# Kernel tuning notes

Measured on AMD Instinct MI355X. Metric: run time of the kernel, lower is better.

## Reference

```python
import jax, jax.numpy as jnp
import numpy as np
from jax import lax

NUM_WORDS, WORD_DIM = 50000, 300
NUM_CHARS, CHAR_DIM = 100, 100
NUM_POS, POS_DIM = 50, 100
NUM_FILTERS, KERNEL = 100, 3
PRIVACY_TERMS = (3, 7, 11)


def setup_inputs() -> dict:
    key = jax.random.key(0)
    ks = jax.random.split(key, 8)
    bs, ls, cl = 64, 512, 32
    return {
        "input_word": jax.random.randint(ks[0], (bs, ls), 0, NUM_WORDS, dtype=jnp.int64 if jax.config.jax_enable_x64 else jnp.int32),
        "input_char": jax.random.randint(ks[1], (bs, ls, cl), 0, NUM_CHARS),
        "input_pos": jax.random.randint(ks[2], (bs, ls), 0, NUM_POS),
        "word_table": jax.random.normal(ks[3], (NUM_WORDS, WORD_DIM), jnp.float32) * 0.1,
        "char_table": jax.random.normal(ks[4], (NUM_CHARS, CHAR_DIM), jnp.float32) * 0.1,
        "pos_table": jax.random.normal(ks[5], (NUM_POS, POS_DIM), jnp.float32) * 0.1,
        "conv_w": jax.random.normal(ks[6], (NUM_FILTERS, CHAR_DIM, KERNEL), jnp.float32) * 0.05,
        "conv_b": jax.random.normal(ks[7], (NUM_FILTERS,), jnp.float32) * 0.05,
    }


def _dist_feature(input_pos):
    # nearest-privacy-token distance: parallel prefix-min via cummax/cummin scans
    priv = jnp.asarray(PRIVACY_TERMS)
    pri_mask = (input_pos[..., None] == priv).any(-1)           # [bs, ls]
    ls = input_pos.shape[1]
    pos_idx = jnp.arange(ls)                                      # [ls]
    last = lax.cummax(jnp.where(pri_mask, pos_idx, -1000), axis=1)                 # last privacy idx <= j
    nxt = lax.cummin(jnp.where(pri_mask, pos_idx, 1000), axis=1, reverse=True)     # next privacy idx >= j
    dis = jnp.minimum(pos_idx - last, nxt - pos_idx).astype(jnp.float32)
    return dis[..., None]                                         # [bs, ls, 1]


def _char_cnn(char_emb, conv_w, conv_b):
    # char_emb: [bs, ls, cl, char_dim] -> [bs, ls, num_filters]
    bs, ls, cl, cd = char_emb.shape
    x = char_emb.reshape(bs * ls, cl, cd).transpose(0, 2, 1)      # [N, C, L]
    y = lax.conv_general_dilated(x, conv_w, window_strides=(1,),
                                 padding=[(KERNEL - 1, KERNEL - 1)],
                                 dimension_numbers=("NCH", "OIH", "NCH"))
    y = y + conv_b[None, :, None]
    y = jnp.tanh(y.max(axis=2))                                   # max over length, then tanh
    return y.reshape(bs, ls, -1)


def reference(input_word, input_char, input_pos, word_table, char_table, pos_table, conv_w, conv_b):
    dis = _dist_feature(input_pos)
    word = word_table[input_word]                                 # [bs, ls, word_dim]
    char = _char_cnn(char_table[input_char], conv_w, conv_b)      # [bs, ls, num_filters]
    pos = pos_table[input_pos]                                    # [bs, ls, pos_dim]
    return jnp.concatenate([dis, word, char, pos], axis=2)
```

## Files before the change

kernel.cpp:

```cpp
#include <hip/hip_runtime.h>
#include <hip/hip_fp16.h>

#define BS 64
#define LS 512
#define CL 32
#define WD 300
#define NC 100
#define CD 100
#define PD 100
#define NF 100
#define KK 3
#define OPAD 128
#define PROW (KK*OPAD)
#define PBYTES (NC*PROW*2)
#define NV4 (PBYTES/16)
#define OUTD 501
#define TPB 64
#define NTHR 1024
#define NCOPY 640
#define NCHAR 384

typedef _Float16 h2 __attribute__((ext_vector_type(2)));

__global__ void precompute_P(const float* __restrict__ conv_w,
                             const float* __restrict__ char_table,
                             _Float16* __restrict__ P) {
    const int c = blockIdx.x;
    const int k = blockIdx.y;
    const int o = threadIdx.x;
    __shared__ float row[CD];
    if (o < CD) row[o] = char_table[c * CD + o];
    __syncthreads();
    float acc = 0.f;
    if (o < NF) {
        const float* w = conv_w + o * (CD * KK) + k;
        #pragma unroll 4
        for (int i = 0; i < CD; ++i) acc += w[i * KK] * row[i];
    }
    P[(c * KK + k) * OPAD + o] = (_Float16)acc;
}

__global__ __launch_bounds__(NTHR, 8) void main_kernel(
        const int* __restrict__ input_word,
        const int* __restrict__ input_char,
        const int* __restrict__ input_pos,
        const float* __restrict__ word_table,
        const float* __restrict__ pos_table,
        const float* __restrict__ conv_b,
        const _Float16* __restrict__ Pg,
        float* __restrict__ out) {
    __shared__ alignas(16) _Float16 Pl[NC * PROW];
    __shared__ alignas(16) unsigned char s_char[TPB * CL];
    __shared__ unsigned long long s_mask[LS / 64];

    const int tid  = threadIdx.x;
    const int tok0 = blockIdx.x * TPB;

    const uint4* src = (const uint4*)Pg;
    const uint4 s0 = src[tid];
    const uint4 s1 = src[tid + NTHR];
    const uint4 s2 = src[tid + 2 * NTHR];
    const uint4 s3 = src[tid + 3 * NTHR];
    uint4 s4 = {};
    const bool h4 = tid < (NV4 - 4 * NTHR);
    if (h4) s4 = src[tid + 4 * NTHR];

    if (tid < LS) {
        const int p = input_pos[(tok0 >> 9) * LS + tid];
        const bool pm = (p == 3) | (p == 7) | (p == 11);
        const unsigned long long b = __ballot(pm);
        if ((tid & 63) == 0) s_mask[tid >> 6] = b;
    }

    if (tid < (TPB * CL) / 4) {
        const int4 c4 = ((const int4*)(input_char + tok0 * CL))[tid];
        ((unsigned*)s_char)[tid] =
            (unsigned)c4.x | ((unsigned)c4.y << 8) | ((unsigned)c4.z << 16) | ((unsigned)c4.w << 24);
    }

    {
        uint4* dst = (uint4*)Pl;
        dst[tid] = s0;
        dst[tid + NTHR] = s1;
        dst[tid + 2 * NTHR] = s2;
        dst[tid + 3 * NTHR] = s3;
        if (h4) dst[tid + 4 * NTHR] = s4;
    }
    __syncthreads();

    if (tid < NCHAR) {
        const int wid  = tid >> 6;
        const int lane = tid & 63;
        const int l    = lane & 15;
        const char* Pb = (const char*)Pl + l * 16;
        const unsigned* s_cw = (const unsigned*)s_char;

        #pragma unroll 1
        for (int pass = 0; pass < 3; ++pass) {
            const int slot = wid * 3 + pass;
            if (slot < 16) {
                const int tb = slot * 4 + (lane >> 4);
                h2 a0[4], a1[4], m[4];
                #pragma unroll
                for (int i = 0; i < 4; ++i) {
                    a0[i] = (h2)(_Float16)0;
                    a1[i] = (h2)(_Float16)0;
                    m[i]  = (h2)(_Float16)(-60000.f);
                }
                #pragma unroll 2
                for (int w = 0; w < CL / 4; ++w) {
                    const unsigned wd = s_cw[tb * (CL / 4) + w];
                    #pragma unroll
                    for (int b = 0; b < 4; ++b) {
                        const int ca = (int)((wd >> (8 * b)) & 0xFFu) * (PROW * 2);
                        const uint4 r0 = *(const uint4*)(Pb + ca + 0 * (OPAD * 2));
                        const uint4 r1 = *(const uint4*)(Pb + ca + 1 * (OPAD * 2));
                        const uint4 r2 = *(const uint4*)(Pb + ca + 2 * (OPAD * 2));
                        #pragma unroll
                        for (int i = 0; i < 4; ++i) {
                            const unsigned c0 = (i == 0) ? r0.x : (i == 1) ? r0.y : (i == 2) ? r0.z : r0.w;
                            const unsigned c1 = (i == 0) ? r1.x : (i == 1) ? r1.y : (i == 2) ? r1.z : r1.w;
                            const unsigned c2 = (i == 0) ? r2.x : (i == 1) ? r2.y : (i == 2) ? r2.z : r2.w;
                            const h2 p0 = __builtin_bit_cast(h2, c0);
                            const h2 p1 = __builtin_bit_cast(h2, c1);
                            const h2 p2 = __builtin_bit_cast(h2, c2);
                            const h2 y = a0[i] + p2;
                            m[i]  = __builtin_elementwise_max(m[i], y);
                            a0[i] = a1[i] + p1;
                            a1[i] = p0;
                        }
                    }
                }
                if (l < 13) {
                    float mm[8];
                    #pragma unroll
                    for (int i = 0; i < 4; ++i) {
                        const h2 v = __builtin_elementwise_max(m[i], __builtin_elementwise_max(a0[i], a1[i]));
                        mm[2 * i]     = (float)v.x;
                        mm[2 * i + 1] = (float)v.y;
                    }
                    const float4 b0 = *(const float4*)(conv_b + 8 * l);
                    float* outc = out + (size_t)(tok0 + tb) * OUTD + 301 + 8 * l;
                    outc[0] = tanhf(mm[0] + b0.x);
                    outc[1] = tanhf(mm[1] + b0.y);
                    outc[2] = tanhf(mm[2] + b0.z);
                    outc[3] = tanhf(mm[3] + b0.w);
                    if (l < 12) {
                        const float4 b1 = *(const float4*)(conv_b + 8 * l + 4);
                        outc[4] = tanhf(mm[4] + b1.x);
                        outc[5] = tanhf(mm[5] + b1.y);
                        outc[6] = tanhf(mm[6] + b1.z);
                        outc[7] = tanhf(mm[7] + b1.w);
                    }
                }
            }
        }

        for (int i = tid; i < TPB * (PD / 4); i += NCHAR) {
            const int t = i / (PD / 4);
            const int j = i - t * (PD / 4);
            const int p = input_pos[tok0 + t];
            const float4 v = ((const float4*)pos_table)[p * (PD / 4) + j];
            float* o = out + (size_t)(tok0 + t) * OUTD + 401 + 4 * j;
            o[0] = v.x; o[1] = v.y; o[2] = v.z; o[3] = v.w;
        }

        if (tid < TPB) {
            const int j = (tok0 & (LS - 1)) + tid;
            const int wj = j >> 6, bj = j & 63;
            int last = -1000;
            {
                unsigned long long x = s_mask[wj] & ((2ull << bj) - 1ull);
                int w = wj;
                while (true) {
                    if (x) { last = w * 64 + 63 - __clzll(x); break; }
                    if (--w < 0) break;
                    x = s_mask[w];
                }
            }
            int nxt = 1000;
            {
                unsigned long long x = s_mask[wj] & (~0ull << bj);
                int w = wj;
                while (true) {
                    if (x) { nxt = w * 64 + (int)__ffsll((long long)x) - 1; break; }
                    if (++w >= LS / 64) break;
                    x = s_mask[w];
                }
            }
            out[(size_t)(tok0 + tid) * OUTD] = (float)min(j - last, nxt - j);
        }
    } else {
        const int t2 = tid - NCHAR;

        #pragma unroll 2
        for (int i = t2; i < TPB * (WD / 4); i += NCOPY) {
            const int t = i / (WD / 4);
            const int j = i - t * (WD / 4);
            const int w = input_word[tok0 + t];
            const float4 v = ((const float4*)word_table)[(size_t)w * (WD / 4) + j];
            float* o = out + (size_t)(tok0 + t) * OUTD + 1 + 4 * j;
            o[0] = v.x; o[1] = v.y; o[2] = v.z; o[3] = v.w;
        }
    }
}

extern "C" void kernel_launch(void* const* d_in, const int* in_sizes, int n_in,
                              void* d_out, int out_size, void* d_ws, size_t ws_size,
                              hipStream_t stream) {
    const int*   input_word = (const int*)d_in[0];
    const int*   input_char = (const int*)d_in[1];
    const int*   input_pos  = (const int*)d_in[2];
    const float* word_table = (const float*)d_in[3];
    const float* char_table = (const float*)d_in[4];
    const float* pos_table  = (const float*)d_in[5];
    const float* conv_w     = (const float*)d_in[6];
    const float* conv_b     = (const float*)d_in[7];
    float* out = (float*)d_out;

    _Float16* P = (_Float16*)d_ws;

    precompute_P<<<dim3(NC, KK), 128, 0, stream>>>(conv_w, char_table, P);
    main_kernel<<<(BS * LS) / TPB, NTHR, 0, stream>>>(
        input_word, input_char, input_pos, word_table, pos_table, conv_b, P, out);
}
```

Baseline: 39.71 us.

## Rebalance waves: 8 char-CNN waves, 8 copy waves with per-token word gathers

```diff
diff --git a/kernel.cpp b/kernel.cpp
--- a/kernel.cpp
+++ b/kernel.cpp
@@ -17,8 +17,6 @@
 #define OUTD 501
 #define TPB 64
 #define NTHR 1024
-#define NCOPY 640
-#define NCHAR 384
 
 typedef _Float16 h2 __attribute__((ext_vector_type(2)));
 
@@ -55,114 +53,109 @@
 
     const int tid  = threadIdx.x;
     const int tok0 = blockIdx.x * TPB;
-
-    const uint4* src = (const uint4*)Pg;
-    const uint4 s0 = src[tid];
-    const uint4 s1 = src[tid + NTHR];
-    const uint4 s2 = src[tid + 2 * NTHR];
-    const uint4 s3 = src[tid + 3 * NTHR];
-    uint4 s4 = {};
-    const bool h4 = tid < (NV4 - 4 * NTHR);
-    if (h4) s4 = src[tid + 4 * NTHR];
-
-    if (tid < LS) {
+    const int wid  = tid >> 6;
+    const int lane = tid & 63;
+
+    if (wid < 8) {
         const int p = input_pos[(tok0 >> 9) * LS + tid];
         const bool pm = (p == 3) | (p == 7) | (p == 11);
         const unsigned long long b = __ballot(pm);
-        if ((tid & 63) == 0) s_mask[tid >> 6] = b;
+        if (lane == 0) s_mask[wid] = b;
+
+        {
+            const int4 c4 = ((const int4*)(input_char + tok0 * CL))[tid];
+            ((unsigned*)s_char)[tid] =
+                (unsigned)c4.x | ((unsigned)c4.y << 8) | ((unsigned)c4.z << 16) | ((unsigned)c4.w << 24);
+        }
+
+        {
+            const uint4* src = (const uint4*)Pg;
+            uint4* dst = (uint4*)Pl;
+            #pragma unroll 2
+            for (int i = tid; i < NV4; i += 512) dst[i] = src[i];
+        }
+    } else {
+        const int cw = wid - 8;
+        #pragma unroll 2
+        for (int tk = 0; tk < 2; ++tk) {
+            const int t = cw * 8 + tk;
+            const int w = __builtin_amdgcn_readfirstlane(input_word[tok0 + t]);
+            const float4* tb = (const float4*)word_table + (size_t)w * (WD / 4);
+            float* o = out + (size_t)(tok0 + t) * OUTD + 1;
+            const float4 v = tb[lane];
+            o[4 * lane + 0] = v.x; o[4 * lane + 1] = v.y;
+            o[4 * lane + 2] = v.z; o[4 * lane + 3] = v.w;
+            if (lane < (WD / 4) - 64) {
+                const float4 v2 = tb[lane + 64];
+                o[4 * (lane + 64) + 0] = v2.x; o[4 * (lane + 64) + 1] = v2.y;
+                o[4 * (lane + 64) + 2] = v2.z; o[4 * (lane + 64) + 3] = v2.w;
+            }
+        }
     }
 
-    if (tid < (TPB * CL) / 4) {
-        const int4 c4 = ((const int4*)(input_char + tok0 * CL))[tid];
-        ((unsigned*)s_char)[tid] =
-            (unsigned)c4.x | ((unsigned)c4.y << 8) | ((unsigned)c4.z << 16) | ((unsigned)c4.w << 24);
-    }
-
-    {
-        uint4* dst = (uint4*)Pl;
-        dst[tid] = s0;
-        dst[tid + NTHR] = s1;
-        dst[tid + 2 * NTHR] = s2;
-        dst[tid + 3 * NTHR] = s3;
-        if (h4) dst[tid + 4 * NTHR] = s4;
-    }
     __syncthreads();
 
-    if (tid < NCHAR) {
-        const int wid  = tid >> 6;
-        const int lane = tid & 63;
-        const int l    = lane & 15;
+    if (wid < 8) {
+        const int l = lane & 15;
         const char* Pb = (const char*)Pl + l * 16;
         const unsigned* s_cw = (const unsigned*)s_char;
 
         #pragma unroll 1
-        for (int pass = 0; pass < 3; ++pass) {
-            const int slot = wid * 3 + pass;
-            if (slot < 16) {
-                const int tb = slot * 4 + (lane >> 4);
-                h2 a0[4], a1[4], m[4];
+        for (int pass = 0; pass < 2; ++pass) {
+            const int tb = wid * 8 + pass * 4 + (lane >> 4);
+            h2 a0[4], a1[4], m[4];
+            #pragma unroll
+            for (int i = 0; i < 4; ++i) {
+                a0[i] = (h2)(_Float16)0;
+                a1[i] = (h2)(_Float16)0;
+                m[i]  = (h2)(_Float16)(-60000.f);
+            }
+            #pragma unroll 2
+            for (int w = 0; w < CL / 4; ++w) {
+                const unsigned wd = s_cw[tb * (CL / 4) + w];
+                #pragma unroll
+                for (int b = 0; b < 4; ++b) {
+                    const int ca = (int)((wd >> (8 * b)) & 0xFFu) * (PROW * 2);
+                    const uint4 r0 = *(const uint4*)(Pb + ca + 0 * (OPAD * 2));
+                    const uint4 r1 = *(const uint4*)(Pb + ca + 1 * (OPAD * 2));
+                    const uint4 r2 = *(const uint4*)(Pb + ca + 2 * (OPAD * 2));
+                    #pragma unroll
+                    for (int i = 0; i < 4; ++i) {
+                        const unsigned c0 = (i == 0) ? r0.x : (i == 1) ? r0.y : (i == 2) ? r0.z : r0.w;
+                        const unsigned c1 = (i == 0) ? r1.x : (i == 1) ? r1.y : (i == 2) ? r1.z : r1.w;
+                        const unsigned c2 = (i == 0) ? r2.x : (i == 1) ? r2.y : (i == 2) ? r2.z : r2.w;
+                        const h2 p0 = __builtin_bit_cast(h2, c0);
+                        const h2 p1 = __builtin_bit_cast(h2, c1);
+                        const h2 p2 = __builtin_bit_cast(h2, c2);
+                        const h2 y = a0[i] + p2;
+                        m[i]  = __builtin_elementwise_max(m[i], y);
+                        a0[i] = a1[i] + p1;
+                        a1[i] = p0;
+                    }
+                }
+            }
+            if (l < 13) {
+                float mm[8];
                 #pragma unroll
                 for (int i = 0; i < 4; ++i) {
-                    a0[i] = (h2)(_Float16)0;
-                    a1[i] = (h2)(_Float16)0;
-                    m[i]  = (h2)(_Float16)(-60000.f);
-                }
-                #pragma unroll 2
-                for (int w = 0; w < CL / 4; ++w) {
-                    const unsigned wd = s_cw[tb * (CL / 4) + w];
-                    #pragma unroll
-                    for (int b = 0; b < 4; ++b) {
-                        const int ca = (int)((wd >> (8 * b)) & 0xFFu) * (PROW * 2);
-                        const uint4 r0 = *(const uint4*)(Pb + ca + 0 * (OPAD * 2));
-                        const uint4 r1 = *(const uint4*)(Pb + ca + 1 * (OPAD * 2));
-                        const uint4 r2 = *(const uint4*)(Pb + ca + 2 * (OPAD * 2));
-                        #pragma unroll
-                        for (int i = 0; i < 4; ++i) {
-                            const unsigned c0 = (i == 0) ? r0.x : (i == 1) ? r0.y : (i == 2) ? r0.z : r0.w;
-                            const unsigned c1 = (i == 0) ? r1.x : (i == 1) ? r1.y : (i == 2) ? r1.z : r1.w;
-                            const unsigned c2 = (i == 0) ? r2.x : (i == 1) ? r2.y : (i == 2) ? r2.z : r2.w;
-                            const h2 p0 = __builtin_bit_cast(h2, c0);
-                            const h2 p1 = __builtin_bit_cast(h2, c1);
-                            const h2 p2 = __builtin_bit_cast(h2, c2);
-                            const h2 y = a0[i] + p2;
-                            m[i]  = __builtin_elementwise_max(m[i], y);
-                            a0[i] = a1[i] + p1;
-                            a1[i] = p0;
-                        }
-                    }
-                }
-                if (l < 13) {
-                    float mm[8];
-                    #pragma unroll
-                    for (int i = 0; i < 4; ++i) {
-                        const h2 v = __builtin_elementwise_max(m[i], __builtin_elementwise_max(a0[i], a1[i]));
-                        mm[2 * i]     = (float)v.x;
-                        mm[2 * i + 1] = (float)v.y;
-                    }
-                    const float4 b0 = *(const float4*)(conv_b + 8 * l);
-                    float* outc = out + (size_t)(tok0 + tb) * OUTD + 301 + 8 * l;
-                    outc[0] = tanhf(mm[0] + b0.x);
-                    outc[1] = tanhf(mm[1] + b0.y);
-                    outc[2] = tanhf(mm[2] + b0.z);
-                    outc[3] = tanhf(mm[3] + b0.w);
-                    if (l < 12) {
-                        const float4 b1 = *(const float4*)(conv_b + 8 * l + 4);
-                        outc[4] = tanhf(mm[4] + b1.x);
-                        outc[5] = tanhf(mm[5] + b1.y);
-                        outc[6] = tanhf(mm[6] + b1.z);
-                        outc[7] = tanhf(mm[7] + b1.w);
-                    }
-                }
-            }
-        }
-
-        for (int i = tid; i < TPB * (PD / 4); i += NCHAR) {
-            const int t = i / (PD / 4);
-            const int j = i - t * (PD / 4);
-            const int p = input_pos[tok0 + t];
-            const float4 v = ((const float4*)pos_table)[p * (PD / 4) + j];
-            float* o = out + (size_t)(tok0 + t) * OUTD + 401 + 4 * j;
-            o[0] = v.x; o[1] = v.y; o[2] = v.z; o[3] = v.w;
+                    const h2 v = __builtin_elementwise_max(m[i], __builtin_elementwise_max(a0[i], a1[i]));
+                    mm[2 * i]     = (float)v.x;
+                    mm[2 * i + 1] = (float)v.y;
+                }
+                const float4 b0 = *(const float4*)(conv_b + 8 * l);
+                float* outc = out + (size_t)(tok0 + tb) * OUTD + 301 + 8 * l;
+                outc[0] = tanhf(mm[0] + b0.x);
+                outc[1] = tanhf(mm[1] + b0.y);
+                outc[2] = tanhf(mm[2] + b0.z);
+                outc[3] = tanhf(mm[3] + b0.w);
+                if (l < 12) {
+                    const float4 b1 = *(const float4*)(conv_b + 8 * l + 4);
+                    outc[4] = tanhf(mm[4] + b1.x);
+                    outc[5] = tanhf(mm[5] + b1.y);
+                    outc[6] = tanhf(mm[6] + b1.z);
+                    outc[7] = tanhf(mm[7] + b1.w);
+                }
+            }
         }
 
         if (tid < TPB) {
@@ -191,16 +184,33 @@
             out[(size_t)(tok0 + tid) * OUTD] = (float)min(j - last, nxt - j);
         }
     } else {
-        const int t2 = tid - NCHAR;
+        const int cw = wid - 8;
 
         #pragma unroll 2
-        for (int i = t2; i < TPB * (WD / 4); i += NCOPY) {
-            const int t = i / (WD / 4);
-            const int j = i - t * (WD / 4);
-            const int w = input_word[tok0 + t];
-            const float4 v = ((const float4*)word_table)[(size_t)w * (WD / 4) + j];
-            float* o = out + (size_t)(tok0 + t) * OUTD + 1 + 4 * j;
-            o[0] = v.x; o[1] = v.y; o[2] = v.z; o[3] = v.w;
+        for (int tk = 2; tk < 8; ++tk) {
+            const int t = cw * 8 + tk;
+            const int w = __builtin_amdgcn_readfirstlane(input_word[tok0 + t]);
+            const float4* tb = (const float4*)word_table + (size_t)w * (WD / 4);
+            float* o = out + (size_t)(tok0 + t) * OUTD + 1;
+            const float4 v = tb[lane];
+            o[4 * lane + 0] = v.x; o[4 * lane + 1] = v.y;
+            o[4 * lane + 2] = v.z; o[4 * lane + 3] = v.w;
+            if (lane < (WD / 4) - 64) {
+                const float4 v2 = tb[lane + 64];
+                o[4 * (lane + 64) + 0] = v2.x; o[4 * (lane + 64) + 1] = v2.y;
+                o[4 * (lane + 64) + 2] = v2.z; o[4 * (lane + 64) + 3] = v2.w;
+            }
+        }
+
+        #pragma unroll 2
+        for (int tk = 0; tk < 8; ++tk) {
+            const int t = cw * 8 + tk;
+            const int p = __builtin_amdgcn_readfirstlane(input_pos[tok0 + t]);
+            if (lane < PD / 4) {
+                const float4 v = ((const float4*)pos_table)[p * (PD / 4) + lane];
+                float* o = out + (size_t)(tok0 + t) * OUTD + 401 + 4 * lane;
+                o[0] = v.x; o[1] = v.y; o[2] = v.z; o[3] = v.w;
+            }
         }
     }
 }
```

Measured after the change: 40.06 us. No clear change (+0.9%).
